# Kernel tuning notes

Hardware: AMD Instinct MI355X
Metric: run time of the kernel (lower is better)

Reference implementation:

```python
import jax, jax.numpy as jnp
import numpy as np

WINDOW = 8  # outlier_fraction = 0.125 -> 1 fp column kept per 8-wide window

# XnorBinaryLinear's STEBinary: sign in fwd, identity (straight-through) in bwd
@jax.custom_vjp
def ste_sign(x):
    return jnp.sign(x)

def _ste_fwd(x):
    return jnp.sign(x), None

def _ste_bwd(_, g):
    return (g,)

ste_sign.defvjp(_ste_fwd, _ste_bwd)


def quant_weight(w):
    # XnorBinaryLinear.quant_weight: per-row mean-center, sign, rescale by
    # detached per-row mean absolute value
    mu = jnp.mean(w, axis=-1, keepdims=True)
    wc = w - mu
    scale = jax.lax.stop_gradient(jnp.mean(jnp.abs(wc), axis=-1, keepdims=True))
    return ste_sign(wc) * scale


def binarize_except_outliers(w):
    # Binarize weight, then restore the max-|w| element of each flat 8-wide
    # window to full precision (calibration = argmax of |w| per window,
    # identical to outlier_calibration with L1 metric on first forward).
    wq = quant_weight(w)
    wv = w.reshape(-1, WINDOW)             # [n_windows, 8]
    idx = jnp.argmax(jnp.abs(wv), axis=1)  # [n_windows] outlier column per window
    mask = jnp.arange(WINDOW)[None, :] == idx[:, None]  # one-hot bool mask
    out = jnp.where(mask, wv, wq.reshape(-1, WINDOW))
    return out.reshape(w.shape)


def setup_inputs() -> dict:
    key = jax.random.key(0)
    k1, k2, k3 = jax.random.split(key, 3)
    x = jax.random.normal(k1, (4, 2048, 4096), dtype=jnp.float32)
    weight = jax.random.normal(k2, (4096, 4096), dtype=jnp.float32) * 0.02
    bias = jax.random.normal(k3, (4096,), dtype=jnp.float32) * 0.02
    return {"x": x, "weight": weight, "bias": bias}


def reference(x, weight, bias):
    w = binarize_except_outliers(weight)     # [OC, IC]
    return jnp.einsum('bsi,oi->bso', x, w) + bias
```

## Files before the change

kernel.cpp:

```cpp
#include <hip/hip_runtime.h>
#include <stdint.h>

#define M_DIM 8192
#define N_DIM 4096
#define K_DIM 4096

#define BM 256
#define BN 256
#define BK 64
#define NT (K_DIM / BK)

typedef float v4f __attribute__((ext_vector_type(4)));
typedef __bf16 v8bf __attribute__((ext_vector_type(8)));

typedef __attribute__((address_space(3))) uint32_t lds_u32_t;
typedef const __attribute__((address_space(1))) uint32_t glb_u32_t;

__device__ inline uint16_t f2bf(float f) {
    union { float f; uint32_t u; } v; v.f = f;
    uint32_t r = v.u + 0x7fffu + ((v.u >> 16) & 1u);
    return (uint16_t)(r >> 16);
}

__global__ __launch_bounds__(256) void cvt_x(const float* __restrict__ x,
                                             uint16_t* __restrict__ xb,
                                             long long n4) {
    long long stride = (long long)gridDim.x * 256;
    for (long long i = (long long)blockIdx.x * 256 + threadIdx.x; i < n4; i += stride) {
        float4 a = ((const float4*)x)[i];
        union { uint16_t h[4]; uint2 u; } o;
        o.h[0] = f2bf(a.x); o.h[1] = f2bf(a.y); o.h[2] = f2bf(a.z); o.h[3] = f2bf(a.w);
        ((uint2*)xb)[i] = o.u;
    }
}

__global__ __launch_bounds__(256) void make_weff(const float* __restrict__ w,
                                                 uint16_t* __restrict__ weff) {
    __shared__ double red[4];
    int row  = blockIdx.x;
    int tid  = threadIdx.x;
    int lane = tid & 63;
    int wid  = tid >> 6;

    const float* wr = w + (size_t)row * K_DIM;
    const float4* w4 = (const float4*)wr + tid * 4;
    float4 r0 = w4[0], r1 = w4[1], r2 = w4[2], r3 = w4[3];
    float v[16] = { r0.x, r0.y, r0.z, r0.w, r1.x, r1.y, r1.z, r1.w,
                    r2.x, r2.y, r2.z, r2.w, r3.x, r3.y, r3.z, r3.w };

    double s = 0.0;
#pragma unroll
    for (int j = 0; j < 16; j++) s += (double)v[j];
#pragma unroll
    for (int off = 32; off > 0; off >>= 1) s += __shfl_down(s, off);
    if (lane == 0) red[wid] = s;
    __syncthreads();
    double mu = (red[0] + red[1] + red[2] + red[3]) * (1.0 / 4096.0);
    __syncthreads();

    double sa = 0.0;
#pragma unroll
    for (int j = 0; j < 16; j++) sa += fabs((double)v[j] - mu);
#pragma unroll
    for (int off = 32; off > 0; off >>= 1) sa += __shfl_down(sa, off);
    if (lane == 0) red[wid] = sa;
    __syncthreads();
    double scale = (red[0] + red[1] + red[2] + red[3]) * (1.0 / 4096.0);

    float scf = (float)scale;
    union { uint16_t h[16]; uint4 u[2]; } o;
#pragma unroll
    for (int w2 = 0; w2 < 2; w2++) {
        int base = w2 * 8;
        int amax = 0;
        float mx = fabsf(v[base]);
#pragma unroll
        for (int j = 1; j < 8; j++) {
            float aj = fabsf(v[base + j]);
            if (aj > mx) { mx = aj; amax = j; }
        }
#pragma unroll
        for (int j = 0; j < 8; j++) {
            double wc = (double)v[base + j] - mu;
            float q = (wc > 0.0) ? scf : ((wc < 0.0) ? -scf : 0.0f);
            o.h[base + j] = f2bf((j == amax) ? v[base + j] : q);
        }
    }
    uint4* dst = (uint4*)(weff + (size_t)row * K_DIM + (size_t)tid * 16);
    dst[0] = o.u[0];
    dst[1] = o.u[1];
}


__device__ inline void async_cp16(const uint16_t* g, uint16_t* lds_uniform) {
    __builtin_amdgcn_global_load_lds((glb_u32_t*)g, (lds_u32_t*)lds_uniform, 16, 0, 0);
}

__device__ __forceinline__ void load4(v8bf (&d)[4], const uint16_t* base) {
#pragma unroll
    for (int i = 0; i < 4; ++i) d[i] = *(const v8bf*)(base + i * 512);
}

template<int MH>
__device__ __forceinline__ void mfma16(v4f (&acc)[8][4], const v8bf (&a)[4], const v8bf (&b)[4]) {
#pragma unroll
    for (int fm = 0; fm < 4; ++fm)
#pragma unroll
        for (int fn = 0; fn < 4; ++fn)
            acc[MH * 4 + fm][fn] =
                __builtin_amdgcn_mfma_f32_16x16x32_bf16(a[fm], b[fn], acc[MH * 4 + fm][fn], 0, 0, 0);
}

#define SB   __builtin_amdgcn_sched_barrier(0)
#define BAR  __builtin_amdgcn_s_barrier()
#define PRIO1 __builtin_amdgcn_s_setprio(1)
#define PRIO0 __builtin_amdgcn_s_setprio(0)
#define VMWAIT(N) asm volatile("s_waitcnt vmcnt(" #N ")" ::: "memory")
#define NOPW ((void)0)

#define STG_A(BUFV, KHV, KOFF) do { \
    async_cp16(a_s0 + (KOFF) + (KHV) * 32, ldsA + ((BUFV) * 2 + (KHV)) * 8192 + wid * 1024);       \
    async_cp16(a_s1 + (KOFF) + (KHV) * 32, ldsA + ((BUFV) * 2 + (KHV)) * 8192 + wid * 1024 + 512); \
} while (0)
#define STG_B(BUFV, KHV, KOFF) do { \
    async_cp16(b_s0 + (KOFF) + (KHV) * 32, ldsB + ((BUFV) * 2 + (KHV)) * 8192 + wid * 1024);       \
    async_cp16(b_s1 + (KOFF) + (KHV) * 32, ldsB + ((BUFV) * 2 + (KHV)) * 8192 + wid * 1024 + 512); \
} while (0)

#define TILE(BUFV, PF1, PF2, WQ1, WQ3, KN1, KN2)                               \
  {                                                                            \
    v8bf a_f[4], b0[4], b1[4];                                                 \
                                                            \
    load4(a_f, rdA + ((BUFV) * 2 + 0) * 8192 + 0 * 2048);                      \
    load4(b0,  rdB + ((BUFV) * 2 + 0) * 8192);                                 \
    if (PF1) { STG_A(1 - (BUFV), 1, KN1); }                                    \
    SB; BAR; SB;                                                               \
    PRIO1; mfma16<0>(acc, a_f, b0); PRIO0;                                     \
    SB; BAR;                                                                   \
                                                            \
    load4(a_f, rdA + ((BUFV) * 2 + 0) * 8192 + 1 * 2048);                      \
    if (PF1) { STG_B(1 - (BUFV), 1, KN1); }                                    \
    WQ1; SB; BAR; SB;                                                          \
    PRIO1; mfma16<1>(acc, a_f, b0); PRIO0;                                     \
    SB; BAR;                                                                   \
                                                            \
    load4(a_f, rdA + ((BUFV) * 2 + 1) * 8192 + 1 * 2048);                      \
    load4(b1,  rdB + ((BUFV) * 2 + 1) * 8192);                                 \
    if (PF2) { STG_A((BUFV), 0, KN2); }                                        \
    SB; BAR; SB;                                                               \
    PRIO1; mfma16<1>(acc, a_f, b1); PRIO0;                                     \
    SB; BAR;                                                                   \
                                                            \
    load4(a_f, rdA + ((BUFV) * 2 + 1) * 8192 + 0 * 2048);                      \
    if (PF2) { STG_B((BUFV), 0, KN2); }                                        \
    WQ3; SB; BAR; SB;                                                          \
    PRIO1; mfma16<0>(acc, a_f, b1); PRIO0;                                     \
    SB; BAR;                                                                   \
  }

__global__ __launch_bounds__(512, 2) void gemm_bt(const uint16_t* __restrict__ A,
                                                  const uint16_t* __restrict__ B,
                                                  const float* __restrict__ bias,
                                                  float* __restrict__ C) {
    __shared__ __attribute__((aligned(128))) uint16_t ldsA[4 * 8192];
    __shared__ __attribute__((aligned(128))) uint16_t ldsB[4 * 8192];

    int tid  = threadIdx.x;
    int lane = tid & 63;
    int wid  = tid >> 6;
    int wm   = wid >> 2;
    int wn   = wid & 3;

    int bid = blockIdx.x;
    int swz = (bid & 7) * 64 + (bid >> 3);
    long long bm = (long long)(swz >> 4) * BM;
    long long bn = (long long)(swz & 15) * BN;

    int srow = lane >> 2;
    int scs  = (lane & 3) ^ ((srow >> 1) & 3);
    const uint16_t* a_s0 = A + (size_t)(bm + wid * 32 +  0 + srow) * K_DIM + scs * 8;
    const uint16_t* a_s1 = A + (size_t)(bm + wid * 32 + 16 + srow) * K_DIM + scs * 8;
    const uint16_t* b_s0 = B + (size_t)(bn + wid * 32 +  0 + srow) * K_DIM + scs * 8;
    const uint16_t* b_s1 = B + (size_t)(bn + wid * 32 + 16 + srow) * K_DIM + scs * 8;

    int rl   = lane & 15;
    int aoff = rl * 32 + (((lane >> 4) ^ ((rl >> 1) & 3)) * 8);
    const uint16_t* rdA = ldsA + wm * 4096 + aoff;
    const uint16_t* rdB = ldsB + wn * 2048 + aoff;

    v4f acc[8][4];
#pragma unroll
    for (int i = 0; i < 8; ++i)
#pragma unroll
        for (int j = 0; j < 4; ++j) acc[i][j] = (v4f)(0.0f);

    STG_A(0, 0, 0); STG_B(0, 0, 0); STG_A(0, 1, 0); STG_B(0, 1, 0);
    STG_A(1, 0, 64); STG_B(1, 0, 64);
    VMWAIT(8); SB; BAR;

#pragma clang loop unroll(disable)
    for (int it = 0; it < NT / 2 - 1; ++it) {
        int t2 = it * 2;
        TILE(0, 1, 1, VMWAIT(8), VMWAIT(8), (t2 + 1) * 64, (t2 + 2) * 64);
        TILE(1, 1, 1, VMWAIT(8), VMWAIT(8), (t2 + 2) * 64, (t2 + 3) * 64);
    }
    TILE(0, 1, 0, VMWAIT(8), VMWAIT(4), (NT - 1) * 64, 0);
    TILE(1, 0, 0, VMWAIT(0), NOPW, 0, 0);

    int cl = lane & 15;
    int ch = lane >> 4;
#pragma unroll
    for (int fn = 0; fn < 4; ++fn) {
        int n = (int)bn + wn * 64 + fn * 16 + cl;
        float bj = bias[n];
#pragma unroll
        for (int m8 = 0; m8 < 8; ++m8) {
            size_t rbase = (size_t)(bm + wm * 128 + m8 * 16 + ch * 4) * N_DIM + n;
#pragma unroll
            for (int g = 0; g < 4; ++g)
                C[rbase + (size_t)g * N_DIM] = acc[m8][fn][g] + bj;
        }
    }
}

extern "C" void kernel_launch(void* const* d_in, const int* in_sizes, int n_in,
                              void* d_out, int out_size, void* d_ws, size_t ws_size,
                              hipStream_t stream) {
    const float* x    = (const float*)d_in[0];
    const float* w    = (const float*)d_in[1];
    const float* bias = (const float*)d_in[2];
    float* out = (float*)d_out;

    uint16_t* xb   = (uint16_t*)d_ws;
    uint16_t* weff = (uint16_t*)((char*)d_ws + (size_t)M_DIM * K_DIM * 2);

    long long n4 = (long long)M_DIM * K_DIM / 4;
    cvt_x<<<dim3(4096), dim3(256), 0, stream>>>(x, xb, n4);
    make_weff<<<dim3(N_DIM), dim3(256), 0, stream>>>(w, weff);
    gemm_bt<<<dim3(N_DIM / BN * (M_DIM / BM)), dim3(512), 0, stream>>>(xb, weff, bias, out);
}
```

Baseline: 536.8 us.

## Double-buffer LDS fragment registers to overlap reads with MFMA phases

Splits the A/B register fragments into two ping-pong sets (aX/aY, bX/bY) so each phase's LDS reads for the next MFMA block are issued before the current MFMA block, including preloading the next tile's first fragments at the end of the previous tile. This aims to hide ds_read latency behind matrix instructions instead of waiting after each barrier. It raises VGPR pressure under launch_bounds(512,2) and relies on the barrier placement to keep LDS reads ordered after the async copies land.

```diff
diff --git a/kernel.cpp b/kernel.cpp
--- a/kernel.cpp
+++ b/kernel.cpp
@@ -127,35 +127,40 @@
     async_cp16(b_s1 + (KOFF) + (KHV) * 32, ldsB + ((BUFV) * 2 + (KHV)) * 8192 + wid * 1024 + 512); \
 } while (0)
 
-#define TILE(BUFV, PF1, PF2, WQ1, WQ3, KN1, KN2)                               \
+#define TILE(BUFV, PF1, PF2, WQ1, WQ3, KN1, KN2, EARLY3)                       \
   {                                                                            \
-    v8bf a_f[4], b0[4], b1[4];                                                 \
-                                                            \
-    load4(a_f, rdA + ((BUFV) * 2 + 0) * 8192 + 0 * 2048);                      \
-    load4(b0,  rdB + ((BUFV) * 2 + 0) * 8192);                                 \
+                                                            \
+    load4(aY, rdA + ((BUFV) * 2 + 0) * 8192 + 1 * 2048);        \
     if (PF1) { STG_A(1 - (BUFV), 1, KN1); }                                    \
     SB; BAR; SB;                                                               \
-    PRIO1; mfma16<0>(acc, a_f, b0); PRIO0;                                     \
-    SB; BAR;                                                                   \
-                                                            \
-    load4(a_f, rdA + ((BUFV) * 2 + 0) * 8192 + 1 * 2048);                      \
+    PRIO1; mfma16<0>(acc, aX, bX); PRIO0;                                      \
+    SB; BAR; SB;                                                               \
+                                                            \
     if (PF1) { STG_B(1 - (BUFV), 1, KN1); }                                    \
-    WQ1; SB; BAR; SB;                                                          \
-    PRIO1; mfma16<1>(acc, a_f, b0); PRIO0;                                     \
-    SB; BAR;                                                                   \
-                                                            \
-    load4(a_f, rdA + ((BUFV) * 2 + 1) * 8192 + 1 * 2048);                      \
-    load4(b1,  rdB + ((BUFV) * 2 + 1) * 8192);                                 \
+    WQ1;                                                                       \
+    SB; BAR; SB;                                                               \
+    load4(aX, rdA + ((BUFV) * 2 + 1) * 8192 + 1 * 2048);        \
+    load4(bY, rdB + ((BUFV) * 2 + 1) * 8192);                       \
+    SB;                                                                        \
+    PRIO1; mfma16<1>(acc, aY, bX); PRIO0;                                      \
+    SB; BAR; SB;                                                               \
+                                                            \
+    load4(aY, rdA + ((BUFV) * 2 + 1) * 8192 + 0 * 2048);        \
     if (PF2) { STG_A((BUFV), 0, KN2); }                                        \
     SB; BAR; SB;                                                               \
-    PRIO1; mfma16<1>(acc, a_f, b1); PRIO0;                                     \
-    SB; BAR;                                                                   \
-                                                            \
-    load4(a_f, rdA + ((BUFV) * 2 + 1) * 8192 + 0 * 2048);                      \
+    PRIO1; mfma16<1>(acc, aX, bY); PRIO0;                                      \
+    SB; BAR; SB;                                                               \
+                                                            \
     if (PF2) { STG_B((BUFV), 0, KN2); }                                        \
-    WQ3; SB; BAR; SB;                                                          \
-    PRIO1; mfma16<0>(acc, a_f, b1); PRIO0;                                     \
-    SB; BAR;                                                                   \
+    WQ3;                                                                       \
+    SB; BAR; SB;                                                               \
+    if (EARLY3) {                                                              \
+        load4(aX, rdA + ((1 - (BUFV)) * 2 + 0) * 8192 + 0 * 2048);             \
+        load4(bX, rdB + ((1 - (BUFV)) * 2 + 0) * 8192);                        \
+    }                                                                          \
+    SB;                                                                        \
+    PRIO1; mfma16<0>(acc, aY, bY); PRIO0;                                      \
+    SB; BAR; SB;                                                               \
   }
 
 __global__ __launch_bounds__(512, 2) void gemm_bt(const uint16_t* __restrict__ A,
@@ -194,18 +199,22 @@
 #pragma unroll
         for (int j = 0; j < 4; ++j) acc[i][j] = (v4f)(0.0f);
 
+    v8bf aX[4], aY[4], bX[4], bY[4];
+
     STG_A(0, 0, 0); STG_B(0, 0, 0); STG_A(0, 1, 0); STG_B(0, 1, 0);
     STG_A(1, 0, 64); STG_B(1, 0, 64);
-    VMWAIT(8); SB; BAR;
+    VMWAIT(8); SB; BAR; SB;
+    load4(aX, rdA + 0 * 8192 + 0 * 2048);
+    load4(bX, rdB + 0 * 8192);
 
 #pragma clang loop unroll(disable)
     for (int it = 0; it < NT / 2 - 1; ++it) {
         int t2 = it * 2;
-        TILE(0, 1, 1, VMWAIT(8), VMWAIT(8), (t2 + 1) * 64, (t2 + 2) * 64);
-        TILE(1, 1, 1, VMWAIT(8), VMWAIT(8), (t2 + 2) * 64, (t2 + 3) * 64);
-    }
-    TILE(0, 1, 0, VMWAIT(8), VMWAIT(4), (NT - 1) * 64, 0);
-    TILE(1, 0, 0, VMWAIT(0), NOPW, 0, 0);
+        TILE(0, 1, 1, VMWAIT(8), VMWAIT(8), (t2 + 1) * 64, (t2 + 2) * 64, 1);
+        TILE(1, 1, 1, VMWAIT(8), VMWAIT(8), (t2 + 2) * 64, (t2 + 3) * 64, 1);
+    }
+    TILE(0, 1, 0, VMWAIT(8), VMWAIT(4), (NT - 1) * 64, 0, 1);
+    TILE(1, 0, 0, VMWAIT(0), NOPW, 0, 0, 0);
 
     int cl = lane & 15;
     int ch = lane >> 4;
```

Result: faster. 525.5 us (-2.1%).

## Shrink GEMM tile to 256x128x32 with simple double-buffered loop and higher occupancy

Applied to the files above, without the earlier changes.

Replaces the 256x256x64 tile and its hand-scheduled four-phase pipeline with a 256x128 tile, BK=32 and a plain double buffer. Each stage issues the next tile's async copies, runs 16 MFMAs per wave, then waits for all loads and hits one barrier. Launch bounds move from 2 to 4 blocks per CU with half the LDS and accumulators. This trades data reuse and overlap for occupancy. The full vmcnt(0) wait each stage and the lower arithmetic intensity can expose memory latency.

```diff
diff --git a/kernel.cpp b/kernel.cpp
--- a/kernel.cpp
+++ b/kernel.cpp
@@ -6,8 +6,8 @@
 #define K_DIM 4096
 
 #define BM 256
-#define BN 256
-#define BK 64
+#define BN 128
+#define BK 32
 #define NT (K_DIM / BK)
 
 typedef float v4f __attribute__((ext_vector_type(4)));
@@ -101,111 +101,86 @@
     for (int i = 0; i < 4; ++i) d[i] = *(const v8bf*)(base + i * 512);
 }
 
-template<int MH>
-__device__ __forceinline__ void mfma16(v4f (&acc)[8][4], const v8bf (&a)[4], const v8bf (&b)[4]) {
-#pragma unroll
-    for (int fm = 0; fm < 4; ++fm)
-#pragma unroll
-        for (int fn = 0; fn < 4; ++fn)
-            acc[MH * 4 + fm][fn] =
-                __builtin_amdgcn_mfma_f32_16x16x32_bf16(a[fm], b[fn], acc[MH * 4 + fm][fn], 0, 0, 0);
-}
-
-#define SB   __builtin_amdgcn_sched_barrier(0)
 #define BAR  __builtin_amdgcn_s_barrier()
 #define PRIO1 __builtin_amdgcn_s_setprio(1)
 #define PRIO0 __builtin_amdgcn_s_setprio(0)
 #define VMWAIT(N) asm volatile("s_waitcnt vmcnt(" #N ")" ::: "memory")
-#define NOPW ((void)0)
-
-#define STG_A(BUFV, KHV, KOFF) do { \
-    async_cp16(a_s0 + (KOFF) + (KHV) * 32, ldsA + ((BUFV) * 2 + (KHV)) * 8192 + wid * 1024);       \
-    async_cp16(a_s1 + (KOFF) + (KHV) * 32, ldsA + ((BUFV) * 2 + (KHV)) * 8192 + wid * 1024 + 512); \
+
+#define STG_A(BUFV, KOFF) do { \
+    async_cp16(a_s0 + (KOFF), ldsA + (BUFV) * 8192 + wid * 1024);       \
+    async_cp16(a_s1 + (KOFF), ldsA + (BUFV) * 8192 + wid * 1024 + 512); \
 } while (0)
-#define STG_B(BUFV, KHV, KOFF) do { \
-    async_cp16(b_s0 + (KOFF) + (KHV) * 32, ldsB + ((BUFV) * 2 + (KHV)) * 8192 + wid * 1024);       \
-    async_cp16(b_s1 + (KOFF) + (KHV) * 32, ldsB + ((BUFV) * 2 + (KHV)) * 8192 + wid * 1024 + 512); \
+#define STG_B(BUFV, KOFF) do { \
+    async_cp16(b_s0 + (KOFF), ldsB + (BUFV) * 4096 + wid * 512);        \
 } while (0)
 
-#define TILE(BUFV, PF1, PF2, WQ1, WQ3, KN1, KN2)                               \
+#define TILE1(BUFV, KNEXT)                                                     \
   {                                                                            \
-    v8bf a_f[4], b0[4], b1[4];                                                 \
-                                                            \
-    load4(a_f, rdA + ((BUFV) * 2 + 0) * 8192 + 0 * 2048);                      \
-    load4(b0,  rdB + ((BUFV) * 2 + 0) * 8192);                                 \
-    if (PF1) { STG_A(1 - (BUFV), 1, KN1); }                                    \
-    SB; BAR; SB;                                                               \
-    PRIO1; mfma16<0>(acc, a_f, b0); PRIO0;                                     \
-    SB; BAR;                                                                   \
-                                                            \
-    load4(a_f, rdA + ((BUFV) * 2 + 0) * 8192 + 1 * 2048);                      \
-    if (PF1) { STG_B(1 - (BUFV), 1, KN1); }                                    \
-    WQ1; SB; BAR; SB;                                                          \
-    PRIO1; mfma16<1>(acc, a_f, b0); PRIO0;                                     \
-    SB; BAR;                                                                   \
-                                                            \
-    load4(a_f, rdA + ((BUFV) * 2 + 1) * 8192 + 1 * 2048);                      \
-    load4(b1,  rdB + ((BUFV) * 2 + 1) * 8192);                                 \
-    if (PF2) { STG_A((BUFV), 0, KN2); }                                        \
-    SB; BAR; SB;                                                               \
-    PRIO1; mfma16<1>(acc, a_f, b1); PRIO0;                                     \
-    SB; BAR;                                                                   \
-                                                            \
-    load4(a_f, rdA + ((BUFV) * 2 + 1) * 8192 + 0 * 2048);                      \
-    if (PF2) { STG_B((BUFV), 0, KN2); }                                        \
-    WQ3; SB; BAR; SB;                                                          \
-    PRIO1; mfma16<0>(acc, a_f, b1); PRIO0;                                     \
-    SB; BAR;                                                                   \
+    v8bf aF[4], bF[4];                                                         \
+    load4(aF, rdA + (BUFV) * 8192);                                            \
+    load4(bF, rdB + (BUFV) * 4096);                                            \
+    STG_A(1 - (BUFV), KNEXT);                                                  \
+    STG_B(1 - (BUFV), KNEXT);                                                  \
+    PRIO1;                                                                     \
+    _Pragma("unroll")                                                          \
+    for (int fm = 0; fm < 4; ++fm)                                             \
+      _Pragma("unroll")                                                        \
+      for (int fn = 0; fn < 4; ++fn)                                           \
+        acc[fm][fn] = __builtin_amdgcn_mfma_f32_16x16x32_bf16(aF[fm], bF[fn],  \
+                                                              acc[fm][fn], 0, 0, 0); \
+    PRIO0;                                                                     \
+    VMWAIT(0);                                                                 \
+    BAR;                                                                       \
   }
 
-__global__ __launch_bounds__(512, 2) void gemm_bt(const uint16_t* __restrict__ A,
+__global__ __launch_bounds__(512, 4) void gemm_bt(const uint16_t* __restrict__ A,
                                                   const uint16_t* __restrict__ B,
                                                   const float* __restrict__ bias,
                                                   float* __restrict__ C) {
-    __shared__ __attribute__((aligned(128))) uint16_t ldsA[4 * 8192];
-    __shared__ __attribute__((aligned(128))) uint16_t ldsB[4 * 8192];
+    __shared__ __attribute__((aligned(128))) uint16_t ldsA[2 * 8192];
+    __shared__ __attribute__((aligned(128))) uint16_t ldsB[2 * 4096];
 
     int tid  = threadIdx.x;
     int lane = tid & 63;
     int wid  = tid >> 6;
-    int wm   = wid >> 2;
-    int wn   = wid & 3;
+    int wm   = wid >> 1;
+    int wn   = wid & 1;
 
     int bid = blockIdx.x;
-    int swz = (bid & 7) * 64 + (bid >> 3);
-    long long bm = (long long)(swz >> 4) * BM;
-    long long bn = (long long)(swz & 15) * BN;
+    int swz = (bid & 7) * 128 + (bid >> 3);
+    long long bm = (long long)(swz >> 5) * BM;
+    long long bn = (long long)(swz & 31) * BN;
 
     int srow = lane >> 2;
     int scs  = (lane & 3) ^ ((srow >> 1) & 3);
     const uint16_t* a_s0 = A + (size_t)(bm + wid * 32 +  0 + srow) * K_DIM + scs * 8;
     const uint16_t* a_s1 = A + (size_t)(bm + wid * 32 + 16 + srow) * K_DIM + scs * 8;
-    const uint16_t* b_s0 = B + (size_t)(bn + wid * 32 +  0 + srow) * K_DIM + scs * 8;
-    const uint16_t* b_s1 = B + (size_t)(bn + wid * 32 + 16 + srow) * K_DIM + scs * 8;
+    const uint16_t* b_s0 = B + (size_t)(bn + wid * 16 +       srow) * K_DIM + scs * 8;
 
     int rl   = lane & 15;
     int aoff = rl * 32 + (((lane >> 4) ^ ((rl >> 1) & 3)) * 8);
-    const uint16_t* rdA = ldsA + wm * 4096 + aoff;
+    const uint16_t* rdA = ldsA + wm * 2048 + aoff;
     const uint16_t* rdB = ldsB + wn * 2048 + aoff;
 
-    v4f acc[8][4];
-#pragma unroll
-    for (int i = 0; i < 8; ++i)
+    v4f acc[4][4];
+#pragma unroll
+    for (int i = 0; i < 4; ++i)
 #pragma unroll
         for (int j = 0; j < 4; ++j) acc[i][j] = (v4f)(0.0f);
 
-    STG_A(0, 0, 0); STG_B(0, 0, 0); STG_A(0, 1, 0); STG_B(0, 1, 0);
-    STG_A(1, 0, 64); STG_B(1, 0, 64);
-    VMWAIT(8); SB; BAR;
+    STG_A(0, 0);
+    STG_B(0, 0);
+    VMWAIT(0);
+    BAR;
 
 #pragma clang loop unroll(disable)
-    for (int it = 0; it < NT / 2 - 1; ++it) {
+    for (int it = 0; it < NT / 2; ++it) {
         int t2 = it * 2;
-        TILE(0, 1, 1, VMWAIT(8), VMWAIT(8), (t2 + 1) * 64, (t2 + 2) * 64);
-        TILE(1, 1, 1, VMWAIT(8), VMWAIT(8), (t2 + 2) * 64, (t2 + 3) * 64);
-    }
-    TILE(0, 1, 0, VMWAIT(8), VMWAIT(4), (NT - 1) * 64, 0);
-    TILE(1, 0, 0, VMWAIT(0), NOPW, 0, 0);
+        int k1 = (t2 + 1) * BK;
+        int k2 = (t2 + 2 < NT) ? (t2 + 2) * BK : t2 * BK;
+        TILE1(0, k1);
+        TILE1(1, k2);
+    }
 
     int cl = lane & 15;
     int ch = lane >> 4;
@@ -214,11 +189,11 @@
         int n = (int)bn + wn * 64 + fn * 16 + cl;
         float bj = bias[n];
 #pragma unroll
-        for (int m8 = 0; m8 < 8; ++m8) {
-            size_t rbase = (size_t)(bm + wm * 128 + m8 * 16 + ch * 4) * N_DIM + n;
+        for (int fm = 0; fm < 4; ++fm) {
+            size_t rbase = (size_t)(bm + wm * 64 + fm * 16 + ch * 4) * N_DIM + n;
 #pragma unroll
             for (int g = 0; g < 4; ++g)
-                C[rbase + (size_t)g * N_DIM] = acc[m8][fn][g] + bj;
+                C[rbase + (size_t)g * N_DIM] = acc[fm][fn][g] + bj;
         }
     }
 }
@@ -237,5 +212,5 @@
     long long n4 = (long long)M_DIM * K_DIM / 4;
     cvt_x<<<dim3(4096), dim3(256), 0, stream>>>(x, xb, n4);
     make_weff<<<dim3(N_DIM), dim3(256), 0, stream>>>(w, weff);
-    gemm_bt<<<dim3(N_DIM / BN * (M_DIM / BM)), dim3(512), 0, stream>>>(xb, weff, bias, out);
-}
+    gemm_bt<<<dim3((M_DIM / BM) * (N_DIM / BN)), dim3(512), 0, stream>>>(xb, weff, bias, out);
+}
```

After: 549.6 us. +2.4%, slower.
